# Optimization experiments

Hardware: AMD Instinct MI355X
Metric: run time of the kernel (lower is better)

Reference implementation:

```python
import jax, jax.numpy as jnp
import numpy as np
from jax import lax

DIM = 1024      # model dim
DS = 16         # d_state
DC = 4          # d_conv
EXP = 2
DI = DIM * EXP  # d_inner = 2048
B, L = 2, 1024


def setup_inputs() -> dict:
    key = jax.random.key(0)
    ks = jax.random.split(key, 10)
    s = lambda k, shape, sc: jax.random.normal(k, shape, jnp.float32) * sc
    return {
        "x": s(ks[0], (B, L, DIM), 1.0),
        "norm_w": jnp.ones((DIM,), jnp.float32),
        "norm_b": jnp.zeros((DIM,), jnp.float32),
        "in_proj_w": s(ks[1], (2 * DI, DIM), DIM ** -0.5),
        "conv_w": s(ks[2], (DI, 1, DC), DC ** -0.5),   # depthwise: (out=DI, in/groups=1, K)
        "conv_b": jnp.zeros((DI,), jnp.float32),
        "x_proj_w": s(ks[3], (2 * DS + 1, DI), DI ** -0.5),
        "dt_w": s(ks[4], (DI, 1), 1.0),
        "dt_b": jax.random.uniform(ks[5], (DI,), jnp.float32, -0.001, 0.001),
        "A_log": s(ks[6], (DI, DS), 1.0),              # self.A (randn); A = -exp(A_log)
        "D_skip": jnp.ones((DI,), jnp.float32),
        "out_proj_w": s(ks[7], (DIM, DI), DI ** -0.5),
    }


def _ssm(x, x_proj_w, dt_w, dt_b, A_log, D_skip):
    # x: (B, L, DI)
    xp = jnp.einsum('bli,pi->blp', x, x_proj_w)            # (B, L, 2*DS+1)
    delta = jax.nn.softplus(xp[..., :1] * dt_w[:, 0] + dt_b)  # (B, L, DI)
    Bp = xp[..., 1:DS + 1]                                  # (B, L, DS)
    Cp = xp[..., DS + 1:]                                   # (B, L, DS)
    A = -jnp.exp(A_log)                                     # (DI, DS)
    dA = jnp.exp(delta[..., None] * A)                      # (B, L, DI, DS)
    dB = delta[..., None] * Bp[:, :, None, :] * x[..., None]  # (B, L, DI, DS)

    def step(h, inp):
        dA_t, dB_t, C_t = inp                               # (B,DI,DS),(B,DI,DS),(B,DS)
        h = dA_t * h + dB_t
        return h, jnp.einsum('bdn,bn->bd', h, C_t)

    h0 = jnp.zeros((x.shape[0], DI, DS), x.dtype)
    _, ys = lax.scan(step, h0, (jnp.swapaxes(dA, 0, 1),
                                jnp.swapaxes(dB, 0, 1),
                                jnp.swapaxes(Cp, 0, 1)))
    y = jnp.swapaxes(ys, 0, 1)                              # (B, L, DI)
    return y + x * D_skip


def reference(x, norm_w, norm_b, in_proj_w, conv_w, conv_b,
              x_proj_w, dt_w, dt_b, A_log, D_skip, out_proj_w):
    # LayerNorm
    mu = x.mean(-1, keepdims=True)
    var = ((x - mu) ** 2).mean(-1, keepdims=True)
    xn = (x - mu) * lax.rsqrt(var + 1e-5) * norm_w + norm_b
    # input projection and gate split
    xz = jnp.einsum('bld,pd->blp', xn, in_proj_w)           # (B, L, 2*DI)
    xi, z = xz[..., :DI], xz[..., DI:]
    # causal depthwise conv (torch pads K-1 both sides then slices [:L] == left-pad K-1)
    xc = lax.conv_general_dilated(jnp.swapaxes(xi, 1, 2), conv_w, (1,),
                                  [(DC - 1, 0)], feature_group_count=DI,
                                  dimension_numbers=('NCH', 'OIH', 'NCH'))
    xc = jnp.swapaxes(xc + conv_b[None, :, None], 1, 2)     # (B, L, DI)
    xc = jax.nn.silu(xc)
    y = _ssm(xc, x_proj_w, dt_w, dt_b, A_log, D_skip)
    y = y * jax.nn.silu(z)
    return x + jnp.einsum('bli,di->bld', y, out_proj_w)
```

## Files before the change

### kernel.cpp

```cpp
#include <hip/hip_runtime.h>
#include <stdint.h>

#define BATCH 2
#define SEQ   1024
#define DIM_  1024
#define DS_   16
#define DI_   2048
#define NTOK  (BATCH*SEQ)
#define NSEG  32
#define LSEG  (SEQ/NSEG)

typedef unsigned short u16;
using s16x8 = __attribute__((ext_vector_type(8))) short;
using f32x4 = __attribute__((ext_vector_type(4))) float;
using u16x4 = __attribute__((ext_vector_type(4))) unsigned short;
using u16x8 = __attribute__((ext_vector_type(8))) unsigned short;

__device__ __forceinline__ float bf2f(u16 u) {
  union { unsigned int i; float f; } c; c.i = ((unsigned int)u) << 16; return c.f;
}
__device__ __forceinline__ u16 f2bf(float f) {
  union { float f; unsigned int i; } c; c.f = f;
  unsigned int r = c.i + 0x7fffu + ((c.i >> 16) & 1u);
  return (u16)(r >> 16);
}
__device__ __forceinline__ float softplus_f(float x) {
  return (x > 15.f) ? x : __logf(1.f + __expf(x));
}
__device__ __forceinline__ u16x4 f4_to_bf(float4 v) {
  u16x4 r; r[0] = f2bf(v.x); r[1] = f2bf(v.y); r[2] = f2bf(v.z); r[3] = f2bf(v.w);
  return r;
}

#define N4_INW  (2 * DI_ * DIM_ / 4)
#define N4_OUTW (DIM_ * DI_ / 4)
#define CVT_BLOCKS ((N4_INW + N4_OUTW + 32768) / 256)
__global__ __launch_bounds__(256) void cvt_ln_kernel(const float* __restrict__ in_w,
    const float* __restrict__ out_w, const float* __restrict__ xproj_w,
    const float* __restrict__ x, const float* __restrict__ nw,
    const float* __restrict__ nb, u16* __restrict__ in_w_bf,
    u16* __restrict__ out_w_bf, u16* __restrict__ xpw_bf, u16* __restrict__ xn) {
  int tid = threadIdx.x;
  if (blockIdx.x < CVT_BLOCKS) {
    int i = blockIdx.x * 256 + tid;
    if (i < N4_INW) {
      ((u16x4*)in_w_bf)[i] = f4_to_bf(((const float4*)in_w)[i]);
    } else if (i < N4_INW + N4_OUTW) {
      int j = i - N4_INW;
      ((u16x4*)out_w_bf)[j] = f4_to_bf(((const float4*)out_w)[j]);
    } else {
      int j = i - (N4_INW + N4_OUTW);
      if (j >= 32768) return;
      int p = (j * 4) >> 11;
      u16x4 r;
      if (p < 33) r = f4_to_bf(((const float4*)xproj_w)[j]);
      else { r[0] = 0; r[1] = 0; r[2] = 0; r[3] = 0; }
      ((u16x4*)xpw_bf)[j] = r;
    }
    return;
  }
  int t = blockIdx.x - CVT_BLOCKS;
  const float* row = x + (size_t)t * DIM_;
  float4 v = ((const float4*)row)[tid];
  float f[4] = {v.x, v.y, v.z, v.w};
  float s = 0.f, sq = 0.f;
#pragma unroll
  for (int j = 0; j < 4; j++) { s += f[j]; sq += f[j] * f[j]; }
#pragma unroll
  for (int m = 1; m < 64; m <<= 1) { s += __shfl_xor(s, m); sq += __shfl_xor(sq, m); }
  __shared__ float rs_[4], rq_[4];
  int wv = tid >> 6;
  if ((tid & 63) == 0) { rs_[wv] = s; rq_[wv] = sq; }
  __syncthreads();
  s = rs_[0] + rs_[1] + rs_[2] + rs_[3];
  sq = rq_[0] + rq_[1] + rq_[2] + rq_[3];
  float mu = s * (1.0f / DIM_);
  float var = sq * (1.0f / DIM_) - mu * mu;
  float rstd = rsqrtf(var + 1e-5f);
  float4 wn = ((const float4*)nw)[tid];
  float4 bn = ((const float4*)nb)[tid];
  u16x4 o;
  o[0] = f2bf((f[0] - mu) * rstd * wn.x + bn.x);
  o[1] = f2bf((f[1] - mu) * rstd * wn.y + bn.y);
  o[2] = f2bf((f[2] - mu) * rstd * wn.z + bn.z);
  o[3] = f2bf((f[3] - mu) * rstd * wn.w + bn.w);
  *(u16x4*)(xn + (size_t)t * DIM_ + tid * 4) = o;
}

template<int TBM, int TBN, int BK, typename OUT, int EPI, int KSPLIT = 1, int SWZ = 0>
__global__ __launch_bounds__(256) void gemm_bt(const u16* __restrict__ A,
    const u16* __restrict__ Wt, OUT* __restrict__ C, const float* __restrict__ X,
    int M, int N, int K) {
  constexpr int LDT = BK + 8;
  constexpr int TPR = BK / 8;
  constexpr int RPP = 256 / TPR;
  constexpr int ALn = TBM / RPP;
  constexpr int BLn = TBN / RPP;
  constexpr int KK = BK / 32;
  constexpr int WM = TBM / 2, WN = TBN / 2;
  constexpr int MI = WM / 16, NJ = WN / 16;
  __shared__ __align__(16) u16 sA[TBM * LDT];
  __shared__ __align__(16) u16 sB[TBN * LDT];
  const int tid = threadIdx.x;
  const int lane = tid & 63, wv = tid >> 6;
  const int wm = (wv >> 1) * WM, wn = (wv & 1) * WN;
  const int bxl = SWZ ? ((blockIdx.x & 7) * (gridDim.x >> 3) + (blockIdx.x >> 3))
                      : blockIdx.x;
  const int bm0 = blockIdx.y * TBM, bn0 = bxl * TBN;
  const int q = lane >> 4, r16 = lane & 15;
  const int srow = tid / TPR, scol = (tid % TPR) * 8;
  const int kc = K / KSPLIT;
  const int k0 = (KSPLIT > 1) ? blockIdx.z * kc : 0;
  const int kend = k0 + kc;

  f32x4 acc[MI][NJ];
#pragma unroll
  for (int i = 0; i < MI; i++)
#pragma unroll
    for (int j = 0; j < NJ; j++)
#pragma unroll
      for (int r = 0; r < 4; r++) acc[i][j][r] = 0.f;

  const u16* Ag = A + (size_t)bm0 * K + scol + k0;
  const u16* Wg = Wt + (size_t)bn0 * K + scol + k0;
  s16x8 ra[ALn], rb[BLn];
#pragma unroll
  for (int i = 0; i < ALn; i++) ra[i] = *(const s16x8*)(Ag + (size_t)(srow + i * RPP) * K);
#pragma unroll
  for (int i = 0; i < BLn; i++) rb[i] = *(const s16x8*)(Wg + (size_t)(srow + i * RPP) * K);

  for (int kt = k0; kt < kend; kt += BK) {
    __syncthreads();
#pragma unroll
    for (int i = 0; i < ALn; i++) *(s16x8*)&sA[(srow + i * RPP) * LDT + scol] = ra[i];
#pragma unroll
    for (int i = 0; i < BLn; i++) *(s16x8*)&sB[(srow + i * RPP) * LDT + scol] = rb[i];
    __syncthreads();
    int kn = kt + BK - k0;
    if (kn < kc) {
#pragma unroll
      for (int i = 0; i < ALn; i++) ra[i] = *(const s16x8*)(Ag + (size_t)(srow + i * RPP) * K + kn);
#pragma unroll
      for (int i = 0; i < BLn; i++) rb[i] = *(const s16x8*)(Wg + (size_t)(srow + i * RPP) * K + kn);
    }
#pragma unroll
    for (int kk = 0; kk < KK; kk++) {
      s16x8 fa[MI], fb[NJ];
#pragma unroll
      for (int i = 0; i < MI; i++)
        fa[i] = *(const s16x8*)&sA[(wm + i * 16 + r16) * LDT + kk * 32 + q * 8];
#pragma unroll
      for (int j = 0; j < NJ; j++)
        fb[j] = *(const s16x8*)&sB[(wn + j * 16 + r16) * LDT + kk * 32 + q * 8];
#pragma unroll
      for (int i = 0; i < MI; i++)
#pragma unroll
        for (int j = 0; j < NJ; j++)
          acc[i][j] = __builtin_amdgcn_mfma_f32_16x16x32_bf16(fa[i], fb[j], acc[i][j], 0, 0, 0);
    }
  }
  OUT* Cz = C + ((KSPLIT > 1) ? (size_t)blockIdx.z * M * N : 0);
#pragma unroll
  for (int i = 0; i < MI; i++)
#pragma unroll
    for (int j = 0; j < NJ; j++) {
      int row0 = bm0 + wm + i * 16 + q * 4;
      int col = bn0 + wn + j * 16 + r16;
#pragma unroll
      for (int r = 0; r < 4; r++) {
        size_t off = (size_t)(row0 + r) * N + col;
        float v = acc[i][j][r];
        if constexpr (EPI == 1) v += X[off];
        if constexpr (sizeof(OUT) == 2) Cz[off] = f2bf(v);
        else                            Cz[off] = v;
      }
    }
}

__global__ __launch_bounds__(256) void convxp_gemm(const u16* __restrict__ xz,
    const float* __restrict__ cw, const float* __restrict__ cb,
    const u16* __restrict__ Wt, float* __restrict__ C, u16* __restrict__ xc) {
  constexpr int BK = 32, LDT = BK + 8;
  constexpr int WM = 32, WN = 32, MI = 2, NJ = 2;
  constexpr int K = DI_, Nn = 64;
  __shared__ __align__(16) u16 sA[64 * LDT];
  __shared__ __align__(16) u16 sB[64 * LDT];
  const int tid = threadIdx.x;
  const int lane = tid & 63, wv = tid >> 6;
  const int wm = (wv >> 1) * WM, wn = (wv & 1) * WN;
  const int bm0 = blockIdx.y * 64;
  const int q = lane >> 4, r16 = lane & 15;
  const int srow = tid >> 2, scol = (tid & 3) * 8;
  const int kc = K / 8;
  const int k0 = blockIdx.z * kc;

  f32x4 acc[MI][NJ];
#pragma unroll
  for (int i = 0; i < MI; i++)
#pragma unroll
    for (int j = 0; j < NJ; j++)
#pragma unroll
      for (int r = 0; r < 4; r++) acc[i][j][r] = 0.f;

  const int tm = bm0 + srow;
  const int l = tm & (SEQ - 1);
  const u16* Wg = Wt + (size_t)srow * K + scol + k0;

  auto conv8 = [&](int kt) -> s16x8 {
    int ch = k0 + kt + scol;
    float a[8];
    float4 cb0 = *(const float4*)(cb + ch);
    float4 cb1 = *(const float4*)(cb + ch + 4);
    a[0] = cb0.x; a[1] = cb0.y; a[2] = cb0.z; a[3] = cb0.w;
    a[4] = cb1.x; a[5] = cb1.y; a[6] = cb1.z; a[7] = cb1.w;
#pragma unroll
    for (int k = 0; k < 4; k++) {
      if (l - 3 + k >= 0) {
        u16x8 v = *(const u16x8*)(xz + (size_t)(tm - 3 + k) * (2 * DI_) + ch);
#pragma unroll
        for (int j = 0; j < 8; j++) {
          float4 wj = ((const float4*)cw)[ch + j];
          float wk = (k == 0) ? wj.x : (k == 1) ? wj.y : (k == 2) ? wj.z : wj.w;
          a[j] = fmaf(bf2f(v[j]), wk, a[j]);
        }
      }
    }
    u16x8 o;
#pragma unroll
    for (int j = 0; j < 8; j++) {
      float s = a[j] / (1.0f + __expf(-a[j]));
      o[j] = f2bf(s);
    }
    *(u16x8*)(xc + (size_t)tm * DI_ + ch) = o;
    return *(s16x8*)&o;
  };

  s16x8 ra = conv8(0);
  s16x8 rb = *(const s16x8*)Wg;

  for (int kt = 0; kt < kc; kt += BK) {
    __syncthreads();
    *(s16x8*)&sA[srow * LDT + scol] = ra;
    *(s16x8*)&sB[srow * LDT + scol] = rb;
    __syncthreads();
    int kn = kt + BK;
    if (kn < kc) {
      ra = conv8(kn);
      rb = *(const s16x8*)(Wg + kn);
    }
    {
      s16x8 fa[MI], fb[NJ];
#pragma unroll
      for (int i = 0; i < MI; i++)
        fa[i] = *(const s16x8*)&sA[(wm + i * 16 + r16) * LDT + q * 8];
#pragma unroll
      for (int j = 0; j < NJ; j++)
        fb[j] = *(const s16x8*)&sB[(wn + j * 16 + r16) * LDT + q * 8];
#pragma unroll
      for (int i = 0; i < MI; i++)
#pragma unroll
        for (int j = 0; j < NJ; j++)
          acc[i][j] = __builtin_amdgcn_mfma_f32_16x16x32_bf16(fa[i], fb[j], acc[i][j], 0, 0, 0);
    }
  }
  float* Cz = C + (size_t)blockIdx.z * NTOK * Nn;
#pragma unroll
  for (int i = 0; i < MI; i++)
#pragma unroll
    for (int j = 0; j < NJ; j++) {
      int row0 = bm0 + wm + i * 16 + q * 4;
      int col = wn + j * 16 + r16;
#pragma unroll
      for (int r = 0; r < 4; r++)
        Cz[(size_t)(row0 + r) * Nn + col] = acc[i][j][r];
    }
}

#define SRT 72
#define XPS 36

__global__ __launch_bounds__(256) void scan_pass1(const float* __restrict__ part,
    const float* __restrict__ dtw, const float* __restrict__ dtb,
    u16* __restrict__ xz, const u16* __restrict__ xc,
    const float* __restrict__ A_log, float* __restrict__ bc,
    float* __restrict__ P, float* __restrict__ Q) {
  __shared__ __align__(16) u16 sD[LSEG * SRT];
  __shared__ __align__(16) u16 sX[LSEG * SRT];
  __shared__ __align__(16) float xps[LSEG][XPS];
  __shared__ float sDr[LSEG];
  int tid = threadIdx.x;
  int lane = tid & 63, wv = tid >> 6;
  int nl = (lane & 3) * 4;
  int dl = wv * 16 + (lane >> 2);
  int d0 = blockIdx.x * 64;
  int s = blockIdx.y, b = blockIdx.z;
  int t0 = b * SEQ + s * LSEG;
  {
    int tr = tid >> 3, c = (tid & 7) * 8;
    *(u16x8*)&sX[tr * SRT + c] = *(const u16x8*)(xc + (size_t)(t0 + tr) * DI_ + d0 + c);
    for (int it = tid; it < LSEG * 33; it += 256) {
      int t = it / 33, c2 = it - t * 33;
      float sum = 0.f;
#pragma unroll
      for (int k = 0; k < 8; k++)
        sum += part[(size_t)k * NTOK * 64 + (size_t)(t0 + t) * 64 + c2];
      if (c2 == 0) sDr[t] = sum;
      else         xps[t][c2 - 1] = sum;
    }
  }
  __syncthreads();
  {
    int t = tid >> 3, c0 = (tid & 7) * 8;
    float dr = sDr[t];
    float w8[8], b8[8];
    *(float4*)w8       = *(const float4*)(dtw + d0 + c0);
    *(float4*)(w8 + 4) = *(const float4*)(dtw + d0 + c0 + 4);
    *(float4*)b8       = *(const float4*)(dtb + d0 + c0);
    *(float4*)(b8 + 4) = *(const float4*)(dtb + d0 + c0 + 4);
    u16x8 o;
#pragma unroll
    for (int j = 0; j < 8; j++) o[j] = f2bf(softplus_f(dr * w8[j] + b8[j]));
    *(u16x8*)&sD[t * SRT + c0] = o;
    *(u16x8*)(xz + (size_t)(t0 + t) * (2 * DI_) + d0 + c0) = o;
    if (blockIdx.x == 0) {
      for (int it = tid; it < LSEG * 32; it += 256) {
        int tt = it >> 5, cc = it & 31;
        bc[(size_t)(t0 + tt) * 32 + cc] = xps[tt][cc];
      }
    }
  }
  int d = d0 + dl;
  float4 Ain = *(const float4*)(A_log + d * DS_ + nl);
  f32x4 Av;
  Av[0] = -__expf(Ain.x); Av[1] = -__expf(Ain.y);
  Av[2] = -__expf(Ain.z); Av[3] = -__expf(Ain.w);
  f32x4 Pv, h;
#pragma unroll
  for (int i = 0; i < 4; i++) { Pv[i] = 1.f; h[i] = 0.f; }
  __syncthreads();
#pragma unroll 8
  for (int j = 0; j < LSEG; j++) {
    float delta = bf2f(sD[j * SRT + dl]);
    float xcv   = bf2f(sX[j * SRT + dl]);
    f32x4 B4 = *(const f32x4*)&xps[j][nl];
    float du = delta * xcv;
#pragma unroll
    for (int i = 0; i < 4; i++) {
      float a = __expf(delta * Av[i]);
      Pv[i] *= a;
      h[i] = fmaf(a, h[i], du * B4[i]);
    }
  }
  size_t idx = ((size_t)((b * NSEG + s) * DI_ + d)) * 16 + nl;
  *(f32x4*)(P + idx) = Pv;
  *(f32x4*)(Q + idx) = h;
}

#define SBC 36
__global__ __launch_bounds__(256) void scan_pass2(const float* __restrict__ bc,
    const u16* __restrict__ dlt, const u16* __restrict__ xc,
    const float* __restrict__ A_log, const float* __restrict__ Dskip,
    const float* __restrict__ P, const float* __restrict__ Q,
    u16* __restrict__ yb) {
  __shared__ __align__(16) u16 sD[LSEG * SRT];
  __shared__ __align__(16) u16 sX[LSEG * SRT];
  __shared__ __align__(16) u16 sZ[LSEG * SRT];
  __shared__ __align__(16) float sB[LSEG * SBC];
  int tid = threadIdx.x;
  int lane = tid & 63, wv = tid >> 6;
  int nl = (lane & 3) * 4;
  int dl = wv * 16 + (lane >> 2);
  int d0 = blockIdx.x * 64;
  int s = blockIdx.y, b = blockIdx.z;
  int t0 = b * SEQ + s * LSEG;
  {
    int tr = tid >> 3, c = (tid & 7) * 8;
    *(u16x8*)&sD[tr * SRT + c] = *(const u16x8*)(dlt + (size_t)(t0 + tr) * (2 * DI_) + d0 + c);
    *(u16x8*)&sZ[tr * SRT + c] = *(const u16x8*)(dlt + (size_t)(t0 + tr) * (2 * DI_) + DI_ + d0 + c);
    *(u16x8*)&sX[tr * SRT + c] = *(const u16x8*)(xc  + (size_t)(t0 + tr) * DI_ + d0 + c);
    int tb = tid & 31, cb = (tid >> 5) * 4;
    *(f32x4*)&sB[tb * SBC + cb] = *(const f32x4*)(bc + (size_t)(t0 + tb) * 32 + cb);
  }
  int d = d0 + dl;
  float4 Ain = *(const float4*)(A_log + d * DS_ + nl);
  f32x4 Av;
  Av[0] = -__expf(Ain.x); Av[1] = -__expf(Ain.y);
  Av[2] = -__expf(Ain.z); Av[3] = -__expf(Ain.w);
  float Dv = Dskip[d];
  f32x4 h;
#pragma unroll
  for (int i = 0; i < 4; i++) h[i] = 0.f;
  for (int s2 = 0; s2 < s; s2++) {
    size_t ix = ((size_t)((b * NSEG + s2) * DI_ + d)) * 16 + nl;
    f32x4 Pv = *(const f32x4*)(P + ix);
    f32x4 Qv = *(const f32x4*)(Q + ix);
#pragma unroll
    for (int i = 0; i < 4; i++) h[i] = fmaf(Pv[i], h[i], Qv[i]);
  }
  __syncthreads();
#pragma unroll 8
  for (int j = 0; j < LSEG; j++) {
    float delta = bf2f(sD[j * SRT + dl]);
    float xcv   = bf2f(sX[j * SRT + dl]);
    f32x4 B4 = *(const f32x4*)&sB[j * SBC + nl];
    f32x4 C4 = *(const f32x4*)&sB[j * SBC + 16 + nl];
    float du = delta * xcv;
#pragma unroll
    for (int i = 0; i < 4; i++) {
      float a = __expf(delta * Av[i]);
      h[i] = fmaf(a, h[i], du * B4[i]);
    }
    float p = h[0] * C4[0];
    p = fmaf(h[1], C4[1], p);
    p = fmaf(h[2], C4[2], p);
    p = fmaf(h[3], C4[3], p);
    p += __shfl_xor(p, 1);
    p += __shfl_xor(p, 2);
    if ((lane & 3) == 0) {
      float z = bf2f(sZ[j * SRT + dl]);
      float sz = z / (1.0f + __expf(-z));
      yb[(size_t)(t0 + j) * DI_ + d] = f2bf((p + xcv * Dv) * sz);
    }
  }
}

extern "C" void kernel_launch(void* const* d_in, const int* in_sizes, int n_in,
                              void* d_out, int out_size, void* d_ws, size_t ws_size,
                              hipStream_t stream) {
  const float* x      = (const float*)d_in[0];
  const float* norm_w = (const float*)d_in[1];
  const float* norm_b = (const float*)d_in[2];
  const float* in_w   = (const float*)d_in[3];
  const float* conv_w = (const float*)d_in[4];
  const float* conv_b = (const float*)d_in[5];
  const float* xproj_w= (const float*)d_in[6];
  const float* dt_w   = (const float*)d_in[7];
  const float* dt_b   = (const float*)d_in[8];
  const float* A_log  = (const float*)d_in[9];
  const float* D_skip = (const float*)d_in[10];
  const float* out_w  = (const float*)d_in[11];
  float* out = (float*)d_out;

  char* ws = (char*)d_ws;
  size_t off = 0;
  auto alloc = [&](size_t bytes) { void* p = ws + off; off += (bytes + 255) & ~255ULL; return p; };
  u16* in_w_bf  = (u16*)alloc((size_t)2 * DI_ * DIM_ * 2);
  u16* out_w_bf = (u16*)alloc((size_t)DIM_ * DI_ * 2);
  u16* xpw_bf   = (u16*)alloc((size_t)64 * DI_ * 2);
  u16* xn       = (u16*)alloc((size_t)NTOK * DIM_ * 2);
  u16* xz       = (u16*)alloc((size_t)NTOK * 2 * DI_ * 2);
  u16* xc       = (u16*)alloc((size_t)NTOK * DI_ * 2);
  float* bc     = (float*)alloc((size_t)NTOK * 32 * 4);
  float* xp_part= (float*)alloc((size_t)8 * NTOK * 64 * 4);
  float* P      = (float*)alloc((size_t)BATCH * NSEG * DI_ * 16 * 4);
  float* Q      = (float*)alloc((size_t)BATCH * NSEG * DI_ * 16 * 4);
  u16* yb       = (u16*)alloc((size_t)NTOK * DI_ * 2);

  cvt_ln_kernel<<<CVT_BLOCKS + NTOK, 256, 0, stream>>>(in_w, out_w, xproj_w, x,
                                                       norm_w, norm_b, in_w_bf,
                                                       out_w_bf, xpw_bf, xn);
  gemm_bt<128, 128, 64, u16, 0, 1, 1><<<dim3((2 * DI_) / 128, NTOK / 128), 256, 0, stream>>>(
      xn, in_w_bf, xz, nullptr, NTOK, 2 * DI_, DIM_);
  convxp_gemm<<<dim3(1, NTOK / 64, 8), 256, 0, stream>>>(
      xz, conv_w, conv_b, xpw_bf, xp_part, xc);
  scan_pass1<<<dim3(DI_ / 64, NSEG, BATCH), 256, 0, stream>>>(
      xp_part, dt_w, dt_b, xz, xc, A_log, bc, P, Q);
  scan_pass2<<<dim3(DI_ / 64, NSEG, BATCH), 256, 0, stream>>>(bc, xz, xc, A_log,
                                                              D_skip, P, Q, yb);
  gemm_bt<64, 64, 64, float, 1, 1, 1><<<dim3(DIM_ / 64, NTOK / 64), 256, 0, stream>>>(
      yb, out_w_bf, out, x, NTOK, DIM_, DI_);
}
```

Baseline: 217.5 us.

## Fuse two-pass chunked scan into single sequential scan kernel with double buffering

Replaces the two-kernel segmented scan (per-segment P/Q summaries plus prefix combine) with one kernel where each block walks all segments of a batch sequentially, prefetching the next segment's inputs into double-buffered shared memory. This removes the P/Q and bc intermediate buffers, one kernel launch, and the redundant recomputation of segment states. In exchange the grid shrinks from thousands of blocks to 64, greatly reducing parallelism and exposing the serial recurrence latency.

```diff
diff --git a/kernel.cpp b/kernel.cpp
--- a/kernel.cpp
+++ b/kernel.cpp
@@ -279,148 +279,101 @@
 #define SRT 72
 #define XPS 36
 
-__global__ __launch_bounds__(256) void scan_pass1(const float* __restrict__ part,
+__global__ __launch_bounds__(256) void scan_full(const float* __restrict__ part,
     const float* __restrict__ dtw, const float* __restrict__ dtb,
-    u16* __restrict__ xz, const u16* __restrict__ xc,
-    const float* __restrict__ A_log, float* __restrict__ bc,
-    float* __restrict__ P, float* __restrict__ Q) {
-  __shared__ __align__(16) u16 sD[LSEG * SRT];
-  __shared__ __align__(16) u16 sX[LSEG * SRT];
-  __shared__ __align__(16) float xps[LSEG][XPS];
-  __shared__ float sDr[LSEG];
+    const u16* __restrict__ xz, const u16* __restrict__ xc,
+    const float* __restrict__ A_log, const float* __restrict__ Dskip,
+    u16* __restrict__ yb) {
+  __shared__ __align__(16) u16 sD[2][LSEG * SRT];
+  __shared__ __align__(16) u16 sX[2][LSEG * SRT];
+  __shared__ __align__(16) u16 sZ[2][LSEG * SRT];
+  __shared__ __align__(16) float xps[2][LSEG][XPS];
+  __shared__ float sDr[2][LSEG];
   int tid = threadIdx.x;
   int lane = tid & 63, wv = tid >> 6;
   int nl = (lane & 3) * 4;
   int dl = wv * 16 + (lane >> 2);
-  int d0 = blockIdx.x * 64;
-  int s = blockIdx.y, b = blockIdx.z;
-  int t0 = b * SEQ + s * LSEG;
-  {
-    int tr = tid >> 3, c = (tid & 7) * 8;
-    *(u16x8*)&sX[tr * SRT + c] = *(const u16x8*)(xc + (size_t)(t0 + tr) * DI_ + d0 + c);
-    for (int it = tid; it < LSEG * 33; it += 256) {
-      int t = it / 33, c2 = it - t * 33;
-      float sum = 0.f;
-#pragma unroll
-      for (int k = 0; k < 8; k++)
-        sum += part[(size_t)k * NTOK * 64 + (size_t)(t0 + t) * 64 + c2];
-      if (c2 == 0) sDr[t] = sum;
-      else         xps[t][c2 - 1] = sum;
-    }
-  }
-  __syncthreads();
-  {
-    int t = tid >> 3, c0 = (tid & 7) * 8;
-    float dr = sDr[t];
-    float w8[8], b8[8];
-    *(float4*)w8       = *(const float4*)(dtw + d0 + c0);
-    *(float4*)(w8 + 4) = *(const float4*)(dtw + d0 + c0 + 4);
-    *(float4*)b8       = *(const float4*)(dtb + d0 + c0);
-    *(float4*)(b8 + 4) = *(const float4*)(dtb + d0 + c0 + 4);
-    u16x8 o;
-#pragma unroll
-    for (int j = 0; j < 8; j++) o[j] = f2bf(softplus_f(dr * w8[j] + b8[j]));
-    *(u16x8*)&sD[t * SRT + c0] = o;
-    *(u16x8*)(xz + (size_t)(t0 + t) * (2 * DI_) + d0 + c0) = o;
-    if (blockIdx.x == 0) {
-      for (int it = tid; it < LSEG * 32; it += 256) {
-        int tt = it >> 5, cc = it & 31;
-        bc[(size_t)(t0 + tt) * 32 + cc] = xps[tt][cc];
-      }
-    }
-  }
+  int d0 = blockIdx.x * 64, b = blockIdx.y;
   int d = d0 + dl;
-  float4 Ain = *(const float4*)(A_log + d * DS_ + nl);
-  f32x4 Av;
-  Av[0] = -__expf(Ain.x); Av[1] = -__expf(Ain.y);
-  Av[2] = -__expf(Ain.z); Av[3] = -__expf(Ain.w);
-  f32x4 Pv, h;
-#pragma unroll
-  for (int i = 0; i < 4; i++) { Pv[i] = 1.f; h[i] = 0.f; }
-  __syncthreads();
-#pragma unroll 8
-  for (int j = 0; j < LSEG; j++) {
-    float delta = bf2f(sD[j * SRT + dl]);
-    float xcv   = bf2f(sX[j * SRT + dl]);
-    f32x4 B4 = *(const f32x4*)&xps[j][nl];
-    float du = delta * xcv;
-#pragma unroll
-    for (int i = 0; i < 4; i++) {
-      float a = __expf(delta * Av[i]);
-      Pv[i] *= a;
-      h[i] = fmaf(a, h[i], du * B4[i]);
-    }
-  }
-  size_t idx = ((size_t)((b * NSEG + s) * DI_ + d)) * 16 + nl;
-  *(f32x4*)(P + idx) = Pv;
-  *(f32x4*)(Q + idx) = h;
-}
-
-#define SBC 36
-__global__ __launch_bounds__(256) void scan_pass2(const float* __restrict__ bc,
-    const u16* __restrict__ dlt, const u16* __restrict__ xc,
-    const float* __restrict__ A_log, const float* __restrict__ Dskip,
-    const float* __restrict__ P, const float* __restrict__ Q,
-    u16* __restrict__ yb) {
-  __shared__ __align__(16) u16 sD[LSEG * SRT];
-  __shared__ __align__(16) u16 sX[LSEG * SRT];
-  __shared__ __align__(16) u16 sZ[LSEG * SRT];
-  __shared__ __align__(16) float sB[LSEG * SBC];
-  int tid = threadIdx.x;
-  int lane = tid & 63, wv = tid >> 6;
-  int nl = (lane & 3) * 4;
-  int dl = wv * 16 + (lane >> 2);
-  int d0 = blockIdx.x * 64;
-  int s = blockIdx.y, b = blockIdx.z;
-  int t0 = b * SEQ + s * LSEG;
-  {
-    int tr = tid >> 3, c = (tid & 7) * 8;
-    *(u16x8*)&sD[tr * SRT + c] = *(const u16x8*)(dlt + (size_t)(t0 + tr) * (2 * DI_) + d0 + c);
-    *(u16x8*)&sZ[tr * SRT + c] = *(const u16x8*)(dlt + (size_t)(t0 + tr) * (2 * DI_) + DI_ + d0 + c);
-    *(u16x8*)&sX[tr * SRT + c] = *(const u16x8*)(xc  + (size_t)(t0 + tr) * DI_ + d0 + c);
-    int tb = tid & 31, cb = (tid >> 5) * 4;
-    *(f32x4*)&sB[tb * SBC + cb] = *(const f32x4*)(bc + (size_t)(t0 + tb) * 32 + cb);
-  }
-  int d = d0 + dl;
+  int tr = tid >> 3, c = (tid & 7) * 8;
+
   float4 Ain = *(const float4*)(A_log + d * DS_ + nl);
   f32x4 Av;
   Av[0] = -__expf(Ain.x); Av[1] = -__expf(Ain.y);
   Av[2] = -__expf(Ain.z); Av[3] = -__expf(Ain.w);
   float Dv = Dskip[d];
+  int dc = (tid & 7) * 8;
+  float w8[8], b8[8];
+  *(float4*)w8       = *(const float4*)(dtw + d0 + dc);
+  *(float4*)(w8 + 4) = *(const float4*)(dtw + d0 + dc + 4);
+  *(float4*)b8       = *(const float4*)(dtb + d0 + dc);
+  *(float4*)(b8 + 4) = *(const float4*)(dtb + d0 + dc + 4);
+
+  auto stage = [&](int buf, int s) {
+    int t0 = b * SEQ + s * LSEG;
+    *(u16x8*)&sX[buf][tr * SRT + c] =
+        *(const u16x8*)(xc + (size_t)(t0 + tr) * DI_ + d0 + c);
+    *(u16x8*)&sZ[buf][tr * SRT + c] =
+        *(const u16x8*)(xz + (size_t)(t0 + tr) * (2 * DI_) + DI_ + d0 + c);
+    for (int it = tid; it < LSEG * 33; it += 256) {
+      int t = it / 33, c2 = it - t * 33;
+      float sum = 0.f;
+#pragma unroll
+      for (int k = 0; k < 8; k++)
+        sum += part[(size_t)k * NTOK * 64 + (size_t)(t0 + t) * 64 + c2];
+      if (c2 == 0) sDr[buf][t] = sum;
+      else         xps[buf][t][c2 - 1] = sum;
+    }
+  };
+  auto dphase = [&](int buf) {
+    int t = tid >> 3;
+    float dr = sDr[buf][t];
+    u16x8 o;
+#pragma unroll
+    for (int j = 0; j < 8; j++) o[j] = f2bf(softplus_f(dr * w8[j] + b8[j]));
+    *(u16x8*)&sD[buf][t * SRT + dc] = o;
+  };
+
+  stage(0, 0);
+  __syncthreads();
+  dphase(0);
+  __syncthreads();
+
   f32x4 h;
 #pragma unroll
   for (int i = 0; i < 4; i++) h[i] = 0.f;
-  for (int s2 = 0; s2 < s; s2++) {
-    size_t ix = ((size_t)((b * NSEG + s2) * DI_ + d)) * 16 + nl;
-    f32x4 Pv = *(const f32x4*)(P + ix);
-    f32x4 Qv = *(const f32x4*)(Q + ix);
-#pragma unroll
-    for (int i = 0; i < 4; i++) h[i] = fmaf(Pv[i], h[i], Qv[i]);
-  }
-  __syncthreads();
+
+  for (int s = 0; s < NSEG; s++) {
+    int cur = s & 1;
+    if (s + 1 < NSEG) stage(cur ^ 1, s + 1);
+    int t0 = b * SEQ + s * LSEG;
 #pragma unroll 8
-  for (int j = 0; j < LSEG; j++) {
-    float delta = bf2f(sD[j * SRT + dl]);
-    float xcv   = bf2f(sX[j * SRT + dl]);
-    f32x4 B4 = *(const f32x4*)&sB[j * SBC + nl];
-    f32x4 C4 = *(const f32x4*)&sB[j * SBC + 16 + nl];
-    float du = delta * xcv;
-#pragma unroll
-    for (int i = 0; i < 4; i++) {
-      float a = __expf(delta * Av[i]);
-      h[i] = fmaf(a, h[i], du * B4[i]);
-    }
-    float p = h[0] * C4[0];
-    p = fmaf(h[1], C4[1], p);
-    p = fmaf(h[2], C4[2], p);
-    p = fmaf(h[3], C4[3], p);
-    p += __shfl_xor(p, 1);
-    p += __shfl_xor(p, 2);
-    if ((lane & 3) == 0) {
-      float z = bf2f(sZ[j * SRT + dl]);
-      float sz = z / (1.0f + __expf(-z));
-      yb[(size_t)(t0 + j) * DI_ + d] = f2bf((p + xcv * Dv) * sz);
-    }
+    for (int j = 0; j < LSEG; j++) {
+      float delta = bf2f(sD[cur][j * SRT + dl]);
+      float xcv   = bf2f(sX[cur][j * SRT + dl]);
+      f32x4 B4 = *(const f32x4*)&xps[cur][j][nl];
+      f32x4 C4 = *(const f32x4*)&xps[cur][j][16 + nl];
+      float du = delta * xcv;
+#pragma unroll
+      for (int i = 0; i < 4; i++) {
+        float a = __expf(delta * Av[i]);
+        h[i] = fmaf(a, h[i], du * B4[i]);
+      }
+      float p = h[0] * C4[0];
+      p = fmaf(h[1], C4[1], p);
+      p = fmaf(h[2], C4[2], p);
+      p = fmaf(h[3], C4[3], p);
+      p += __shfl_xor(p, 1);
+      p += __shfl_xor(p, 2);
+      if ((lane & 3) == 0) {
+        float z = bf2f(sZ[cur][j * SRT + dl]);
+        float sz = z / (1.0f + __expf(-z));
+        yb[(size_t)(t0 + j) * DI_ + d] = f2bf((p + xcv * Dv) * sz);
+      }
+    }
+    __syncthreads();
+    if (s + 1 < NSEG) dphase(cur ^ 1);
+    __syncthreads();
   }
 }
 
@@ -450,10 +403,7 @@
   u16* xn       = (u16*)alloc((size_t)NTOK * DIM_ * 2);
   u16* xz       = (u16*)alloc((size_t)NTOK * 2 * DI_ * 2);
   u16* xc       = (u16*)alloc((size_t)NTOK * DI_ * 2);
-  float* bc     = (float*)alloc((size_t)NTOK * 32 * 4);
   float* xp_part= (float*)alloc((size_t)8 * NTOK * 64 * 4);
-  float* P      = (float*)alloc((size_t)BATCH * NSEG * DI_ * 16 * 4);
-  float* Q      = (float*)alloc((size_t)BATCH * NSEG * DI_ * 16 * 4);
   u16* yb       = (u16*)alloc((size_t)NTOK * DI_ * 2);
 
   cvt_ln_kernel<<<CVT_BLOCKS + NTOK, 256, 0, stream>>>(in_w, out_w, xproj_w, x,
@@ -463,10 +413,8 @@
       xn, in_w_bf, xz, nullptr, NTOK, 2 * DI_, DIM_);
   convxp_gemm<<<dim3(1, NTOK / 64, 8), 256, 0, stream>>>(
       xz, conv_w, conv_b, xpw_bf, xp_part, xc);
-  scan_pass1<<<dim3(DI_ / 64, NSEG, BATCH), 256, 0, stream>>>(
-      xp_part, dt_w, dt_b, xz, xc, A_log, bc, P, Q);
-  scan_pass2<<<dim3(DI_ / 64, NSEG, BATCH), 256, 0, stream>>>(bc, xz, xc, A_log,
-                                                              D_skip, P, Q, yb);
+  scan_full<<<dim3(DI_ / 64, BATCH), 256, 0, stream>>>(
+      xp_part, dt_w, dt_b, xz, xc, A_log, D_skip, yb);
   gemm_bt<64, 64, 64, float, 1, 1, 1><<<dim3(DIM_ / 64, NTOK / 64), 256, 0, stream>>>(
       yb, out_w_bf, out, x, NTOK, DIM_, DI_);
 }
```

Measured after the change: 481.7 us. 2.21x slower.
